# Kernel tuning notes

Measured on AMD Instinct MI355X. Metric: run time of the kernel, lower is better.

The kernel has to match this reference:

```python
import jax, jax.numpy as jnp
import numpy as np

N, E = 50000, 1600000
F_IN, EDGE_DIM, HID, HEADS, NCLS = 64, 16, 128, 4, 40
C = HID // HEADS  # per-head dim = 32


def setup_inputs() -> dict:
    key = jax.random.key(0)
    ks = jax.random.split(key, 20)
    s = 0.1
    inp = {
        'x': jax.random.normal(ks[0], (N, F_IN), jnp.float32),
        'edge_index': jax.random.randint(ks[1], (2, E), 0, N, jnp.int64),
        'edge_attr': jax.random.normal(ks[2], (E, EDGE_DIM), jnp.float32),
        # layer 1 params
        'W1': jax.random.normal(ks[3], (HID, F_IN), jnp.float32) * s,
        'as1': jax.random.normal(ks[4], (HEADS, C), jnp.float32) * s,
        'ad1': jax.random.normal(ks[5], (HEADS, C), jnp.float32) * s,
        'ae1': jax.random.normal(ks[6], (HEADS, C), jnp.float32) * s,
        'We1': jax.random.normal(ks[7], (HID, EDGE_DIM), jnp.float32) * s,
        'b1': jnp.zeros((HID,), jnp.float32),
        # layer 2 params
        'W2': jax.random.normal(ks[8], (HID, HID), jnp.float32) * s,
        'as2': jax.random.normal(ks[9], (HEADS, C), jnp.float32) * s,
        'ad2': jax.random.normal(ks[10], (HEADS, C), jnp.float32) * s,
        'ae2': jax.random.normal(ks[11], (HEADS, C), jnp.float32) * s,
        'We2': jax.random.normal(ks[12], (HID, EDGE_DIM), jnp.float32) * s,
        'b2': jnp.zeros((HID,), jnp.float32),
        # final classifier
        'Wlin': jax.random.normal(ks[13], (NCLS, HID), jnp.float32) * s,
        'blin': jnp.zeros((NCLS,), jnp.float32),
    }
    return inp


def gat_conv(x, src, dst, eattr, W, a_s, a_d, a_e, We, b):
    """PyG GATConv (concat=True, add_self_loops=True, fill_value='mean'), eval mode."""
    n = x.shape[0]
    H, Cd = a_s.shape
    h = (x @ W.T).reshape(n, H, Cd)  # [N,H,C]
    # self-loop edge_attr = per-destination mean of incoming edge_attr
    cnt = jax.ops.segment_sum(jnp.ones((dst.shape[0],), eattr.dtype), dst, num_segments=n)
    mean_ea = jax.ops.segment_sum(eattr, dst, num_segments=n) / jnp.maximum(cnt, 1.0)[:, None]
    loops = jnp.arange(n, dtype=src.dtype)
    s_idx = jnp.concatenate([src, loops])
    d_idx = jnp.concatenate([dst, loops])
    ea = jnp.concatenate([eattr, mean_ea], axis=0)  # [E+N, edge_dim]
    e = (ea @ We.T).reshape(-1, H, Cd)
    # edge-wise attention logits
    alpha = (h * a_s).sum(-1)[s_idx] + (h * a_d).sum(-1)[d_idx] + (e * a_e).sum(-1)  # [E+N,H]
    alpha = jax.nn.leaky_relu(alpha, 0.2)
    # segment softmax over destination neighborhoods (every node has a self-loop)
    amax = jax.ops.segment_max(alpha, d_idx, num_segments=n)
    ex = jnp.exp(alpha - amax[d_idx])
    den = jax.ops.segment_sum(ex, d_idx, num_segments=n)
    coef = ex / (den[d_idx] + 1e-16)
    out = jax.ops.segment_sum(h[s_idx] * coef[:, :, None], d_idx, num_segments=n)
    return out.reshape(n, H * Cd) + b


def reference(x, edge_index, edge_attr, W1, as1, ad1, ae1, We1, b1,
              W2, as2, ad2, ae2, We2, b2, Wlin, blin):
    src, dst = edge_index[0], edge_index[1]
    h = jax.nn.relu(gat_conv(x, src, dst, edge_attr, W1, as1, ad1, ae1, We1, b1))
    h = jax.nn.relu(gat_conv(h, src, dst, edge_attr, W2, as2, ad2, ae2, We2, b2))
    logits = h @ Wlin.T + blin
    return jax.nn.log_softmax(logits, axis=1)
```

## Files before the change

### kernel.cpp

```cpp
#include <hip/hip_runtime.h>
#include <hip/hip_bf16.h>
#include <math.h>


#define CHUNK 2048

typedef __attribute__((ext_vector_type(8))) short short8;
typedef __attribute__((ext_vector_type(4))) float floatx4;
typedef __attribute__((ext_vector_type(2))) float floatx2;

__device__ __forceinline__ unsigned short f2bf(float f) {
  unsigned u = __float_as_uint(f);
  unsigned r = u + 0x7FFFu + ((u >> 16) & 1u);
  return (unsigned short)(r >> 16);
}
__device__ __forceinline__ float bf2f(unsigned short b) {
  return __uint_as_float(((unsigned)b) << 16);
}

__global__ __launch_bounds__(512) void hist_kernel(const int* __restrict__ dst,
                                                   int* __restrict__ bucketCnt,
                                                   int E, int NB) {
  __shared__ int hist[512];
  const int tid = threadIdx.x;
  hist[tid] = 0;
  __syncthreads();
  const int e0 = blockIdx.x * CHUNK, e1 = min(e0 + CHUNK, E);
  for (int e = e0 + tid; e < e1; e += 512) atomicAdd(&hist[dst[e] >> 7], 1);
  __syncthreads();
  if (tid < NB && hist[tid]) atomicAdd(&bucketCnt[tid], hist[tid]);
}

__global__ __launch_bounds__(512) void scanB_kernel(const int* __restrict__ bucketCnt,
                                                    int* __restrict__ bucketOffs,
                                                    int* __restrict__ bucketPos,
                                                    int* __restrict__ offs,
                                                    int NB, int N, int E) {
  __shared__ int sc[512];
  const int tid = threadIdx.x;
  const int v = (tid < NB) ? bucketCnt[tid] : 0;
  sc[tid] = v;
  __syncthreads();
  for (int off = 1; off < 512; off <<= 1) {
    int t = (tid >= off) ? sc[tid - off] : 0;
    __syncthreads();
    sc[tid] += t;
    __syncthreads();
  }
  const int excl = sc[tid] - v;
  if (tid < NB) { bucketOffs[tid] = excl; bucketPos[tid] = excl; }
  if (tid == 0) { bucketOffs[NB] = E; offs[N] = E; }
}

__global__ __launch_bounds__(512) void partB_kernel(const int* __restrict__ src,
                                                    const int* __restrict__ dst,
                                                    const float* __restrict__ ea,
                                                    const float* __restrict__ ae1,
                                                    const float* __restrict__ We1,
                                                    const float* __restrict__ ae2,
                                                    const float* __restrict__ We2,
                                                    int* __restrict__ bucketPos,
                                                    int4* __restrict__ binned16,
                                                    int* __restrict__ binned4,
                                                    unsigned char* __restrict__ dlArr,
                                                    int E, int NB) {
  __shared__ float wa[128];
  __shared__ int hist[512], sc[512], lbase[513], gbase[512], lcnt[512];
  __shared__ int4 stg16[CHUNK];
  __shared__ int stg4[CHUNK];
  __shared__ unsigned char stg1[CHUNK];
  const int tid = threadIdx.x;
  const int e0 = blockIdx.x * CHUNK;
  const int e1 = min(e0 + CHUNK, E);
  hist[tid] = 0; lcnt[tid] = 0;
  if (tid < 128) {
    const float* aev = (tid < 64) ? ae1 : ae2;
    const float* Wev = (tid < 64) ? We1 : We2;
    const int h = (tid >> 4) & 3;
    const int d = tid & 15;
    float s = 0.f;
#pragma unroll
    for (int c = 0; c < 32; ++c) s += aev[h * 32 + c] * Wev[(h * 32 + c) * 16 + d];
    wa[tid] = s;
  }
  __syncthreads();
  for (int e = e0 + tid; e < e1; e += 512) atomicAdd(&hist[dst[e] >> 7], 1);
  __syncthreads();
  sc[tid] = hist[tid];
  __syncthreads();
  for (int off = 1; off < 512; off <<= 1) {
    int t = (tid >= off) ? sc[tid - off] : 0;
    __syncthreads();
    sc[tid] += t;
    __syncthreads();
  }
  lbase[tid + 1] = sc[tid];
  if (tid == 0) lbase[0] = 0;
  if (tid < NB && hist[tid] > 0) gbase[tid] = atomicAdd(&bucketPos[tid], hist[tid]);
  __syncthreads();
  for (int e = e0 + tid; e < e1; e += 512) {
    const int d = dst[e];
    const int b = d >> 7;
    const int lr = atomicAdd(&lcnt[b], 1);
    const float4* p = (const float4*)(ea + (size_t)e * 16);
    float4 q0 = p[0], q1 = p[1], q2 = p[2], q3 = p[3];
    float v16[16] = {q0.x, q0.y, q0.z, q0.w, q1.x, q1.y, q1.z, q1.w,
                     q2.x, q2.y, q2.z, q2.w, q3.x, q3.y, q3.z, q3.w};
    unsigned short rr[8];
#pragma unroll
    for (int h = 0; h < 8; ++h) {
      float s = 0.f;
#pragma unroll
      for (int d2 = 0; d2 < 16; ++d2) s += v16[d2] * wa[h * 16 + d2];
      rr[h] = f2bf(s);
    }
    int4 v;
    v.x = (src[e] & 0xFFFF) | ((d & 127) << 16);
    v.y = (int)(((unsigned)rr[1] << 16) | rr[0]);
    v.z = (int)(((unsigned)rr[3] << 16) | rr[2]);
    v.w = (int)(((unsigned)rr[5] << 16) | rr[4]);
    const int sp = lbase[b] + lr;
    stg16[sp] = v;
    stg4[sp] = (int)(((unsigned)rr[7] << 16) | rr[6]);
    stg1[sp] = (unsigned char)(d & 127);
  }
  __syncthreads();
  const int total = e1 - e0;
  for (int t = tid; t < total; t += 512) {
    int lo = 0, hi = 511;
    while (lo < hi) {
      int mid = (lo + hi + 1) >> 1;
      if (lbase[mid] <= t) lo = mid; else hi = mid - 1;
    }
    const int g = gbase[lo] + (t - lbase[lo]);
    binned16[g] = stg16[t];
    binned4[g] = stg4[t];
    dlArr[g] = stg1[t];
  }
}

__global__ __launch_bounds__(256) void passC_kernel(const int4* __restrict__ binned16,
                                                    const int* __restrict__ binned4,
                                                    const unsigned char* __restrict__ dlArr,
                                                    const int* __restrict__ bucketOffs,
                                                    int* __restrict__ srcS,
                                                    uint2* __restrict__ aeS1,
                                                    uint2* __restrict__ aeS2,
                                                    int* __restrict__ offs, int N) {
  __shared__ int cnt[128], dbase[129], dpos[128];
  const int tid = threadIdx.x;
  const int b = blockIdx.x;
  const int bo = bucketOffs[b], be = bucketOffs[b + 1];
  const int m = be - bo;
  if (tid < 128) { cnt[tid] = 0; dpos[tid] = 0; }
  __syncthreads();
  for (int t = tid; t < m; t += 256) atomicAdd(&cnt[dlArr[bo + t]], 1);
  __syncthreads();
  for (int off = 1; off < 128; off <<= 1) {
    int t = (tid < 128 && tid >= (unsigned)off) ? cnt[tid - off] : 0;
    __syncthreads();
    if (tid < 128) cnt[tid] += t;
    __syncthreads();
  }
  if (tid == 0) dbase[0] = 0;
  if (tid < 128) dbase[tid + 1] = cnt[tid];
  __syncthreads();
  const int dcnt = min(128, N - (b << 7));
  if (tid < dcnt) offs[(b << 7) + tid] = bo + dbase[tid];
  for (int t = tid; t < m; t += 256) {
    const int4 v = binned16[bo + t];
    const int w4 = binned4[bo + t];
    const int dl = (v.x >> 16) & 127;
    const int p = dbase[dl] + atomicAdd(&dpos[dl], 1);
    srcS[bo + p] = v.x & 0xFFFF;
    aeS1[bo + p] = make_uint2((unsigned)v.y, (unsigned)v.z);
    aeS2[bo + p] = make_uint2((unsigned)v.w, (unsigned)w4);
  }
}

__global__ __launch_bounds__(256) void cvtall_kernel(const float* __restrict__ W1,
                                                     unsigned short* __restrict__ Wb1,
                                                     const float* __restrict__ W2,
                                                     unsigned short* __restrict__ Wb2,
                                                     const float* __restrict__ Wlin,
                                                     unsigned short* __restrict__ whi,
                                                     unsigned short* __restrict__ wlo) {
  const int n1 = 128 * 64, n2 = 128 * 128, n3 = 48 * 128;
  int i = blockIdx.x * 256 + threadIdx.x;
  if (i < n1) {
    Wb1[i] = f2bf(W1[i]);
  } else if (i < n1 + n2) {
    Wb2[i - n1] = f2bf(W2[i - n1]);
  } else if (i < n1 + n2 + n3) {
    const int j = i - n1 - n2;
    float v = (j < 40 * 128) ? Wlin[j] : 0.f;
    unsigned short h = f2bf(v);
    whi[j] = h;
    wlo[j] = f2bf(v - bf2f(h));
  }
}

#define GEMM_MFMA_SWAPPED(KTOT, PA, PB)                                            \
  {                                                                                \
    for (int kc = 0; kc < (KTOT); kc += 32) {                                      \
      const int koff = kc + (quad << 3);                                           \
      short8 aw[2], bx[4];                                                         \
      _Pragma("unroll") for (int ct = 0; ct < 2; ++ct)                             \
        aw[ct] = *(const short8*)(&Bs[(w * 32 + ct * 16 + l15) * (PB) + koff]);    \
      _Pragma("unroll") for (int nt_ = 0; nt_ < 4; ++nt_)                          \
        bx[nt_] = *(const short8*)(&As[(nt_ * 16 + l15) * (PA) + koff]);           \
      _Pragma("unroll") for (int ct = 0; ct < 2; ++ct)                             \
        _Pragma("unroll") for (int nt_ = 0; nt_ < 4; ++nt_)                        \
          acc[ct][nt_] =                                                           \
              __builtin_amdgcn_mfma_f32_16x16x32_bf16(aw[ct], bx[nt_],             \
                                                      acc[ct][nt_], 0, 0, 0);      \
    }                                                                              \
  }

#define GEMM_WRITE_H_SWAPPED()                                                     \
  {                                                                                \
    _Pragma("unroll") for (int nt_ = 0; nt_ < 4; ++nt_) {                          \
      const int node = m0 + nt_ * 16 + l15;                                        \
      if (node < n) {                                                              \
        _Pragma("unroll") for (int ct = 0; ct < 2; ++ct) {                         \
          const int ch = w * 32 + ct * 16 + (quad << 2);                           \
          ushort4 o;                                                               \
          o.x = f2bf(acc[ct][nt_][0]); o.y = f2bf(acc[ct][nt_][1]);                \
          o.z = f2bf(acc[ct][nt_][2]); o.w = f2bf(acc[ct][nt_][3]);                \
          *(ushort4*)(H + (size_t)node * 128 + ch) = o;                            \
        }                                                                          \
      }                                                                            \
    }                                                                              \
  }

#define GEMM_SCORE_SWAPPED()                                                       \
  {                                                                                \
    float asv[2][4], adv[2][4];                                                    \
    _Pragma("unroll") for (int ct = 0; ct < 2; ++ct)                               \
      _Pragma("unroll") for (int r = 0; r < 4; ++r) {                              \
        const int c = w * 32 + ct * 16 + (quad << 2) + r;                          \
        asv[ct][r] = a_s[c]; adv[ct][r] = a_d[c];                                  \
      }                                                                            \
    _Pragma("unroll") for (int nt_ = 0; nt_ < 4; ++nt_) {                          \
      float ps = 0.f, pd = 0.f;                                                    \
      _Pragma("unroll") for (int ct = 0; ct < 2; ++ct)                             \
        _Pragma("unroll") for (int r = 0; r < 4; ++r) {                            \
          ps += acc[ct][nt_][r] * asv[ct][r];                                      \
          pd += acc[ct][nt_][r] * adv[ct][r];                                      \
        }                                                                          \
      ps += __shfl_xor(ps, 16); ps += __shfl_xor(ps, 32);                          \
      pd += __shfl_xor(pd, 16); pd += __shfl_xor(pd, 32);                          \
      if (lane < 16) {                                                             \
        const int node = m0 + nt_ * 16 + lane;                                     \
        if (node < n) {                                                            \
          ssc[(size_t)node * 4 + w] = ps;                                          \
          dsc[(size_t)node * 4 + w] = pd;                                          \
        }                                                                          \
      }                                                                            \
    }                                                                              \
  }

__global__ __launch_bounds__(256) void gemm_score_f32_kernel(const float* __restrict__ X,
                                                             const unsigned short* __restrict__ Wb,
                                                             const float* __restrict__ a_s,
                                                             const float* __restrict__ a_d,
                                                             unsigned short* __restrict__ H,
                                                             float* __restrict__ ssc,
                                                             float* __restrict__ dsc,
                                                             int n) {
  __shared__ unsigned short As[64 * 72];
  __shared__ unsigned short Bs[128 * 72];
  const int tid = threadIdx.x;
  const int w = tid >> 6;
  const int lane = tid & 63;
  const int m0 = blockIdx.x * 64;
  const int quad = lane >> 4;
  const int l15 = lane & 15;

#pragma unroll
  for (int it = 0; it < 4; ++it) {
    const int idx = it * 256 + tid;
    const int row = idx >> 4;
    const int c4 = (idx & 15) * 4;
    const int grow = min(m0 + row, n - 1);
    const float4 q = *(const float4*)(X + (size_t)grow * 64 + c4);
    unsigned short* dstp = &As[row * 72 + c4];
    dstp[0] = f2bf(q.x); dstp[1] = f2bf(q.y); dstp[2] = f2bf(q.z); dstp[3] = f2bf(q.w);
  }
#pragma unroll
  for (int it = 0; it < 4; ++it) {
    const int idx = it * 256 + tid;
    const int row = idx >> 3;
    const int c8 = (idx & 7) * 8;
    short8 v = *(const short8*)(Wb + (size_t)row * 64 + c8);
    *(short8*)(&Bs[row * 72 + c8]) = v;
  }
  __syncthreads();

  floatx4 acc[2][4];
#pragma unroll
  for (int ct = 0; ct < 2; ++ct)
#pragma unroll
    for (int nt_ = 0; nt_ < 4; ++nt_) acc[ct][nt_] = (floatx4)(0.f);

  GEMM_MFMA_SWAPPED(64, 72, 72)
  GEMM_WRITE_H_SWAPPED()
  GEMM_SCORE_SWAPPED()
}

__global__ __launch_bounds__(256) void gemm_score_kernel(const unsigned short* __restrict__ X,
                                                         const unsigned short* __restrict__ Wb,
                                                         const float* __restrict__ a_s,
                                                         const float* __restrict__ a_d,
                                                         unsigned short* __restrict__ H,
                                                         float* __restrict__ ssc,
                                                         float* __restrict__ dsc,
                                                         int n) {
  __shared__ unsigned short As[64 * 136];
  __shared__ unsigned short Bs[128 * 136];
  const int tid = threadIdx.x;
  const int w = tid >> 6;
  const int lane = tid & 63;
  const int m0 = blockIdx.x * 64;
  const int quad = lane >> 4;
  const int l15 = lane & 15;

#pragma unroll
  for (int it = 0; it < 4; ++it) {
    const int idx = it * 256 + tid;
    const int row = idx >> 4;
    const int c8 = (idx & 15) * 8;
    const int grow = min(m0 + row, n - 1);
    short8 v = *(const short8*)(X + (size_t)grow * 128 + c8);
    *(short8*)(&As[row * 136 + c8]) = v;
  }
#pragma unroll
  for (int it = 0; it < 8; ++it) {
    const int idx = it * 256 + tid;
    const int row = idx >> 4;
    const int c8 = (idx & 15) * 8;
    short8 v = *(const short8*)(Wb + (size_t)row * 128 + c8);
    *(short8*)(&Bs[row * 136 + c8]) = v;
  }
  __syncthreads();

  floatx4 acc[2][4];
#pragma unroll
  for (int ct = 0; ct < 2; ++ct)
#pragma unroll
    for (int nt_ = 0; nt_ < 4; ++nt_) acc[ct][nt_] = (floatx4)(0.f);

  GEMM_MFMA_SWAPPED(128, 136, 136)
  GEMM_WRITE_H_SWAPPED()
  GEMM_SCORE_SWAPPED()
}

__device__ __forceinline__ float leaky02(float a) { return a > 0.f ? a : 0.2f * a; }
__device__ __forceinline__ float sel4(float4 v, int h) {
  return (h == 0) ? v.x : (h == 1) ? v.y : (h == 2) ? v.z : v.w;
}

__global__ __launch_bounds__(256) void agg_kernel(const unsigned short* __restrict__ hin,
                                                  const float* __restrict__ ssc,
                                                  const float* __restrict__ dsc,
                                                  const unsigned short* __restrict__ aeS,
                                                  const int* __restrict__ offs,
                                                  const int* __restrict__ srcS,
                                                  const float* __restrict__ bias,
                                                  unsigned short* __restrict__ hout, int n) {
  __shared__ int sbuf[4][64];
  __shared__ float pbuf[4][256];
  const int tid = threadIdx.x;
  const int wv = tid >> 6;
  const int lane = tid & 63;
  const int node = blockIdx.x * 4 + wv;
  if (node >= n) return;
  const int l32 = lane & 31;
  const int half = lane >> 5;
  const int ch4 = l32 * 4;
  const int headB = l32 >> 3;
  const float4 dv = *(const float4*)(dsc + (size_t)node * 4);
  float4 l4 = make_float4(0.f, 0.f, 0.f, 0.f);
  float4 sa = make_float4(0.f, 0.f, 0.f, 0.f);
  floatx2 acc01 = (floatx2)(0.f);
  floatx2 acc23 = (floatx2)(0.f);
  const int j0 = offs[node], j1 = offs[node + 1];

  for (int jc = j0; jc < j1; jc += 64) {
    const int len = min(64, j1 - jc);
    float4 p4 = make_float4(0.f, 0.f, 0.f, 0.f);
    int sv = 0;
    if (lane < len) {
      const int j = jc + lane;
      sv = srcS[j];
      const ushort4 aq = *(const ushort4*)(aeS + (size_t)j * 4);
      const float4 ae4 = make_float4(bf2f(aq.x), bf2f(aq.y), bf2f(aq.z), bf2f(aq.w));
      const float4 ss4 = *(const float4*)(ssc + (size_t)sv * 4);
      sa.x += ae4.x; sa.y += ae4.y; sa.z += ae4.z; sa.w += ae4.w;
      p4.x = __expf(leaky02(ss4.x + dv.x + ae4.x));
      p4.y = __expf(leaky02(ss4.y + dv.y + ae4.y));
      p4.z = __expf(leaky02(ss4.z + dv.z + ae4.z));
      p4.w = __expf(leaky02(ss4.w + dv.w + ae4.w));
    }
    sbuf[wv][lane] = sv;
    *(float4*)(&pbuf[wv][lane * 4]) = p4;
    l4.x += p4.x; l4.y += p4.y; l4.z += p4.z; l4.w += p4.w;
    int k = 0;
    for (; k + 8 <= len; k += 8) {
      int s[4];
      float p[4];
      uint2 d[4];
#pragma unroll
      for (int u = 0; u < 4; ++u) {
        const int kk = k + 2 * u + half;
        s[u] = sbuf[wv][kk];
        p[u] = pbuf[wv][kk * 4 + headB];
      }
#pragma unroll
      for (int u = 0; u < 4; ++u)
        d[u] = *(const uint2*)(hin + (size_t)s[u] * 128 + ch4);
#pragma unroll
      for (int u = 0; u < 4; ++u) {
        floatx2 p2; p2.x = p[u]; p2.y = p[u];
        floatx2 h01, h23;
        h01.x = __uint_as_float(d[u].x << 16);
        h01.y = __uint_as_float(d[u].x & 0xFFFF0000u);
        h23.x = __uint_as_float(d[u].y << 16);
        h23.y = __uint_as_float(d[u].y & 0xFFFF0000u);
        acc01 += p2 * h01;
        acc23 += p2 * h23;
      }
    }
    for (; k < len; k += 2) {
      int kk = k + half;
      if (kk < len) {
        int s = sbuf[wv][kk];
        float p = pbuf[wv][kk * 4 + headB];
        uint2 d = *(const uint2*)(hin + (size_t)s * 128 + ch4);
        floatx2 p2; p2.x = p; p2.y = p;
        floatx2 h01, h23;
        h01.x = __uint_as_float(d.x << 16);
        h01.y = __uint_as_float(d.x & 0xFFFF0000u);
        h23.x = __uint_as_float(d.y << 16);
        h23.y = __uint_as_float(d.y & 0xFFFF0000u);
        acc01 += p2 * h01;
        acc23 += p2 * h23;
      }
    }
  }

  float acc[4] = {acc01.x, acc01.y, acc23.x, acc23.y};
#pragma unroll
  for (int off = 32; off; off >>= 1) {
    sa.x += __shfl_xor(sa.x, off);
    sa.y += __shfl_xor(sa.y, off);
    sa.z += __shfl_xor(sa.z, off);
    sa.w += __shfl_xor(sa.w, off);
    l4.x += __shfl_xor(l4.x, off);
    l4.y += __shfl_xor(l4.y, off);
    l4.z += __shfl_xor(l4.z, off);
    l4.w += __shfl_xor(l4.w, off);
  }
#pragma unroll
  for (int i = 0; i < 4; ++i) acc[i] += __shfl_xor(acc[i], 32);

  const int deg = j1 - j0;
  const float invd = 1.f / fmaxf((float)deg, 1.f);
  const float ssn = ssc[(size_t)node * 4 + headB];
  const float aloop = leaky02(ssn + sel4(dv, headB) + sel4(sa, headB) * invd);
  const float pl = __expf(aloop);
  const float lF = sel4(l4, headB) + pl;
  const uint2 hd = *(const uint2*)(hin + (size_t)node * 128 + ch4);
  const float hv0 = __uint_as_float(hd.x << 16);
  const float hv1 = __uint_as_float(hd.x & 0xFFFF0000u);
  const float hv2 = __uint_as_float(hd.y << 16);
  const float hv3 = __uint_as_float(hd.y & 0xFFFF0000u);
  const float inv = 1.f / (lF + 1e-16f);
  const float4 bi = *(const float4*)(bias + ch4);
  const float o0 = fmaxf((acc[0] + pl * hv0) * inv + bi.x, 0.f);
  const float o1 = fmaxf((acc[1] + pl * hv1) * inv + bi.y, 0.f);
  const float o2 = fmaxf((acc[2] + pl * hv2) * inv + bi.z, 0.f);
  const float o3 = fmaxf((acc[3] + pl * hv3) * inv + bi.w, 0.f);
  if (half == 0) {
    ushort4 o;
    o.x = f2bf(o0); o.y = f2bf(o1); o.z = f2bf(o2); o.w = f2bf(o3);
    *(ushort4*)(hout + (size_t)node * 128 + ch4) = o;
  }
}

__global__ __launch_bounds__(256) void classifier_kernel(const unsigned short* __restrict__ h,
                                                         const unsigned short* __restrict__ Whi,
                                                         const unsigned short* __restrict__ Wlo,
                                                         const float* __restrict__ blin,
                                                         float* __restrict__ out, int n) {
  const int w = threadIdx.x >> 6;
  const int lane = threadIdx.x & 63;
  const int quad = lane >> 4;
  const int l15 = lane & 15;
  const int row0 = blockIdx.x * 64 + w * 16;
  if (row0 >= n) return;
  int rowm = row0 + l15;
  if (rowm >= n) rowm = n - 1;
  floatx4 acc[3];
#pragma unroll
  for (int nt = 0; nt < 3; ++nt) acc[nt] = (floatx4)(0.f);
  const size_t hbase = (size_t)rowm * 128;
#pragma unroll
  for (int kc = 0; kc < 128; kc += 32) {
    const int koff = kc + (quad << 3);
    short8 a = *(const short8*)(h + hbase + koff);
#pragma unroll
    for (int nt = 0; nt < 3; ++nt) {
      short8 bh = *(const short8*)(Whi + (size_t)(nt * 16 + l15) * 128 + koff);
      short8 bl = *(const short8*)(Wlo + (size_t)(nt * 16 + l15) * 128 + koff);
      acc[nt] = __builtin_amdgcn_mfma_f32_16x16x32_bf16(a, bh, acc[nt], 0, 0, 0);
      acc[nt] = __builtin_amdgcn_mfma_f32_16x16x32_bf16(a, bl, acc[nt], 0, 0, 0);
    }
  }
  const float bl0 = blin[l15];
  const float bl1 = blin[16 + l15];
  const float bl2 = (l15 < 8) ? blin[32 + l15] : 0.f;
#pragma unroll
  for (int r = 0; r < 4; ++r) {
    const int rrow = row0 + (quad << 2) + r;
    const float v0 = acc[0][r] + bl0;
    const float v1 = acc[1][r] + bl1;
    const float v2 = (l15 < 8) ? (acc[2][r] + bl2) : -INFINITY;
    float m = fmaxf(v0, fmaxf(v1, v2));
#pragma unroll
    for (int off = 8; off; off >>= 1) m = fmaxf(m, __shfl_xor(m, off, 16));
    const float e2 = (l15 < 8) ? __expf(v2 - m) : 0.f;
    float s = __expf(v0 - m) + __expf(v1 - m) + e2;
#pragma unroll
    for (int off = 8; off; off >>= 1) s += __shfl_xor(s, off, 16);
    const float ls = m + __logf(s);
    if (rrow < n) {
      float* po = out + (size_t)rrow * 40;
      po[l15] = v0 - ls;
      po[16 + l15] = v1 - ls;
      if (l15 < 8) po[32 + l15] = v2 - ls;
    }
  }
}

extern "C" void kernel_launch(void* const* d_in, const int* in_sizes, int n_in,
                              void* d_out, int out_size, void* d_ws, size_t ws_size,
                              hipStream_t stream) {
  const float* x    = (const float*)d_in[0];
  const int*   eidx = (const int*)d_in[1];
  const float* ea   = (const float*)d_in[2];
  const float* W1   = (const float*)d_in[3];
  const float* as1  = (const float*)d_in[4];
  const float* ad1  = (const float*)d_in[5];
  const float* ae1w = (const float*)d_in[6];
  const float* We1  = (const float*)d_in[7];
  const float* b1   = (const float*)d_in[8];
  const float* W2   = (const float*)d_in[9];
  const float* as2  = (const float*)d_in[10];
  const float* ad2  = (const float*)d_in[11];
  const float* ae2w = (const float*)d_in[12];
  const float* We2  = (const float*)d_in[13];
  const float* b2   = (const float*)d_in[14];
  const float* Wlin = (const float*)d_in[15];
  const float* blin = (const float*)d_in[16];
  float* out = (float*)d_out;

  const int N = in_sizes[0] / 64;
  const int E = in_sizes[1] / 2;
  const int* src = eidx;
  const int* dst = eidx + E;
  const int NB = (N + 127) >> 7;

  char* wsb = (char*)d_ws;
  size_t off = 0;
  auto alloc = [&](size_t bytes) -> void* {
    void* p = wsb + off;
    off = (off + bytes + 255) & ~(size_t)255;
    return p;
  };
  int* bucketCnt  = (int*)alloc(512 * 4);
  int* bucketOffs = (int*)alloc(513 * 4);
  int* bucketPos  = (int*)alloc(512 * 4);
  int* offs       = (int*)alloc((size_t)(N + 1) * 4);
  uint2* aeS1     = (uint2*)alloc((size_t)E * 8);
  uint2* aeS2     = (uint2*)alloc((size_t)E * 8);
  void* regC      = alloc((size_t)E * 16);
  int4* binned16  = (int4*)regC;
  unsigned short* hA = (unsigned short*)regC;
  int* binned4    = (int*)alloc((size_t)E * 4);
  unsigned char* dlArr = (unsigned char*)alloc((size_t)E);
  int* srcS       = (int*)alloc((size_t)E * 4);
  unsigned short* Wb1 = (unsigned short*)alloc(128 * 64 * 2);
  unsigned short* Wb2 = (unsigned short*)alloc(128 * 128 * 2);
  unsigned short* Wlh = (unsigned short*)alloc(48 * 128 * 2);
  unsigned short* Wll = (unsigned short*)alloc(48 * 128 * 2);
  float* ssc      = (float*)alloc((size_t)N * 4 * 4);
  float* dsc      = (float*)alloc((size_t)N * 4 * 4);
  unsigned short* hB = (unsigned short*)alloc((size_t)N * 128 * 2);

  const int gg = (N + 63) / 64;
  const int gs = (N + 3) / 4;
  const int gp = (E + CHUNK - 1) / CHUNK;
  const int ncvt = 128 * 64 + 128 * 128 + 48 * 128;

  hipMemsetAsync(bucketCnt, 0, 512 * 4, stream);
  hist_kernel<<<gp, 512, 0, stream>>>(dst, bucketCnt, E, NB);
  scanB_kernel<<<1, 512, 0, stream>>>(bucketCnt, bucketOffs, bucketPos, offs, NB, N, E);
  partB_kernel<<<gp, 512, 0, stream>>>(src, dst, ea, ae1w, We1, ae2w, We2, bucketPos,
                                       binned16, binned4, dlArr, E, NB);
  passC_kernel<<<NB, 256, 0, stream>>>(binned16, binned4, dlArr, bucketOffs, srcS,
                                       aeS1, aeS2, offs, N);

  cvtall_kernel<<<(ncvt + 255) / 256, 256, 0, stream>>>(W1, Wb1, W2, Wb2, Wlin, Wlh, Wll);

  gemm_score_f32_kernel<<<gg, 256, 0, stream>>>(x, Wb1, as1, ad1, hA, ssc, dsc, N);
  agg_kernel<<<gs, 256, 0, stream>>>(hA, ssc, dsc, (const unsigned short*)aeS1, offs, srcS, b1, hB, N);

  gemm_score_kernel<<<gg, 256, 0, stream>>>(hB, Wb2, as2, ad2, hA, ssc, dsc, N);
  agg_kernel<<<gs, 256, 0, stream>>>(hA, ssc, dsc, (const unsigned short*)aeS2, offs, srcS, b2, hB, N);

  classifier_kernel<<<gg, 256, 0, stream>>>(hB, Wlh, Wll, blin, out, N);
}
```

Baseline: 464.6 us.

## Reuse per-chunk histograms in partition kernel and encode bucket in packed edge

The histogram kernel now writes each chunk's per-bucket counts to global memory, so the partition kernel no longer recomputes the histogram from dst. The 512-entry block scan is replaced by a wave-level shuffle scan plus a per-wave offset sum, which removes most of the barriers. The bucket id is packed into the upper bits of the staged edge word, so the scatter phase reads it directly instead of binary-searching lbase, and the byte staging array is dropped. In exchange it adds a small global buffer write and read per chunk, and it relies on the bucket id fitting in 9 bits.

```diff
diff --git a/kernel.cpp b/kernel.cpp
--- a/kernel.cpp
+++ b/kernel.cpp
@@ -20,6 +20,7 @@
 
 __global__ __launch_bounds__(512) void hist_kernel(const int* __restrict__ dst,
                                                    int* __restrict__ bucketCnt,
+                                                   int* __restrict__ chunkHist,
                                                    int E, int NB) {
   __shared__ int hist[512];
   const int tid = threadIdx.x;
@@ -28,6 +29,7 @@
   const int e0 = blockIdx.x * CHUNK, e1 = min(e0 + CHUNK, E);
   for (int e = e0 + tid; e < e1; e += 512) atomicAdd(&hist[dst[e] >> 7], 1);
   __syncthreads();
+  chunkHist[(size_t)blockIdx.x * 512 + tid] = hist[tid];
   if (tid < NB && hist[tid]) atomicAdd(&bucketCnt[tid], hist[tid]);
 }
 
@@ -59,20 +61,23 @@
                                                     const float* __restrict__ We1,
                                                     const float* __restrict__ ae2,
                                                     const float* __restrict__ We2,
+                                                    const int* __restrict__ chunkHist,
                                                     int* __restrict__ bucketPos,
                                                     int4* __restrict__ binned16,
                                                     int* __restrict__ binned4,
                                                     unsigned char* __restrict__ dlArr,
                                                     int E, int NB) {
   __shared__ float wa[128];
-  __shared__ int hist[512], sc[512], lbase[513], gbase[512], lcnt[512];
+  __shared__ int lbase[513], gbase[512], lcnt[512];
+  __shared__ int waveSum[8];
   __shared__ int4 stg16[CHUNK];
   __shared__ int stg4[CHUNK];
-  __shared__ unsigned char stg1[CHUNK];
   const int tid = threadIdx.x;
+  const int wv = tid >> 6;
+  const int lane = tid & 63;
   const int e0 = blockIdx.x * CHUNK;
   const int e1 = min(e0 + CHUNK, E);
-  hist[tid] = 0; lcnt[tid] = 0;
+  lcnt[tid] = 0;
   if (tid < 128) {
     const float* aev = (tid < 64) ? ae1 : ae2;
     const float* Wev = (tid < 64) ? We1 : We2;
@@ -83,20 +88,22 @@
     for (int c = 0; c < 32; ++c) s += aev[h * 32 + c] * Wev[(h * 32 + c) * 16 + d];
     wa[tid] = s;
   }
-  __syncthreads();
-  for (int e = e0 + tid; e < e1; e += 512) atomicAdd(&hist[dst[e] >> 7], 1);
-  __syncthreads();
-  sc[tid] = hist[tid];
-  __syncthreads();
-  for (int off = 1; off < 512; off <<= 1) {
-    int t = (tid >= off) ? sc[tid - off] : 0;
-    __syncthreads();
-    sc[tid] += t;
-    __syncthreads();
-  }
-  lbase[tid + 1] = sc[tid];
+  const int hv = chunkHist[(size_t)blockIdx.x * 512 + tid];
+  int v = hv;
+#pragma unroll
+  for (int off = 1; off < 64; off <<= 1) {
+    int t = __shfl_up(v, off);
+    if (lane >= off) v += t;
+  }
+  if (lane == 63) waveSum[wv] = v;
+  __syncthreads();
+  int woff = 0;
+#pragma unroll
+  for (int i = 0; i < 8; ++i) woff += (i < wv) ? waveSum[i] : 0;
+  const int incl = v + woff;
+  lbase[tid + 1] = incl;
   if (tid == 0) lbase[0] = 0;
-  if (tid < NB && hist[tid] > 0) gbase[tid] = atomicAdd(&bucketPos[tid], hist[tid]);
+  if (tid < NB && hv > 0) gbase[tid] = atomicAdd(&bucketPos[tid], hv);
   __syncthreads();
   for (int e = e0 + tid; e < e1; e += 512) {
     const int d = dst[e];
@@ -109,33 +116,30 @@
     unsigned short rr[8];
 #pragma unroll
     for (int h = 0; h < 8; ++h) {
-      float s = 0.f;
-#pragma unroll
-      for (int d2 = 0; d2 < 16; ++d2) s += v16[d2] * wa[h * 16 + d2];
-      rr[h] = f2bf(s);
+      float sm = 0.f;
+#pragma unroll
+      for (int d2 = 0; d2 < 16; ++d2) sm += v16[d2] * wa[h * 16 + d2];
+      rr[h] = f2bf(sm);
     }
-    int4 v;
-    v.x = (src[e] & 0xFFFF) | ((d & 127) << 16);
-    v.y = (int)(((unsigned)rr[1] << 16) | rr[0]);
-    v.z = (int)(((unsigned)rr[3] << 16) | rr[2]);
-    v.w = (int)(((unsigned)rr[5] << 16) | rr[4]);
+    int4 pv;
+    pv.x = (int)(((unsigned)(src[e] & 0xFFFF)) | ((unsigned)(d & 127) << 16) |
+                 ((unsigned)b << 23));
+    pv.y = (int)(((unsigned)rr[1] << 16) | rr[0]);
+    pv.z = (int)(((unsigned)rr[3] << 16) | rr[2]);
+    pv.w = (int)(((unsigned)rr[5] << 16) | rr[4]);
     const int sp = lbase[b] + lr;
-    stg16[sp] = v;
+    stg16[sp] = pv;
     stg4[sp] = (int)(((unsigned)rr[7] << 16) | rr[6]);
-    stg1[sp] = (unsigned char)(d & 127);
   }
   __syncthreads();
   const int total = e1 - e0;
   for (int t = tid; t < total; t += 512) {
-    int lo = 0, hi = 511;
-    while (lo < hi) {
-      int mid = (lo + hi + 1) >> 1;
-      if (lbase[mid] <= t) lo = mid; else hi = mid - 1;
-    }
-    const int g = gbase[lo] + (t - lbase[lo]);
-    binned16[g] = stg16[t];
+    const int4 pv = stg16[t];
+    const int b = (int)(((unsigned)pv.x) >> 23);
+    const int g = gbase[b] + (t - lbase[b]);
+    binned16[g] = pv;
     binned4[g] = stg4[t];
-    dlArr[g] = stg1[t];
+    dlArr[g] = (unsigned char)((pv.x >> 16) & 127);
   }
 }
 
@@ -570,6 +574,7 @@
   const int* src = eidx;
   const int* dst = eidx + E;
   const int NB = (N + 127) >> 7;
+  const int gp = (E + CHUNK - 1) / CHUNK;
 
   char* wsb = (char*)d_ws;
   size_t off = 0;
@@ -582,6 +587,7 @@
   int* bucketOffs = (int*)alloc(513 * 4);
   int* bucketPos  = (int*)alloc(512 * 4);
   int* offs       = (int*)alloc((size_t)(N + 1) * 4);
+  int* chunkHist  = (int*)alloc((size_t)gp * 512 * 4);
   uint2* aeS1     = (uint2*)alloc((size_t)E * 8);
   uint2* aeS2     = (uint2*)alloc((size_t)E * 8);
   void* regC      = alloc((size_t)E * 16);
@@ -600,14 +606,13 @@
 
   const int gg = (N + 63) / 64;
   const int gs = (N + 3) / 4;
-  const int gp = (E + CHUNK - 1) / CHUNK;
   const int ncvt = 128 * 64 + 128 * 128 + 48 * 128;
 
   hipMemsetAsync(bucketCnt, 0, 512 * 4, stream);
-  hist_kernel<<<gp, 512, 0, stream>>>(dst, bucketCnt, E, NB);
+  hist_kernel<<<gp, 512, 0, stream>>>(dst, bucketCnt, chunkHist, E, NB);
   scanB_kernel<<<1, 512, 0, stream>>>(bucketCnt, bucketOffs, bucketPos, offs, NB, N, E);
-  partB_kernel<<<gp, 512, 0, stream>>>(src, dst, ea, ae1w, We1, ae2w, We2, bucketPos,
-                                       binned16, binned4, dlArr, E, NB);
+  partB_kernel<<<gp, 512, 0, stream>>>(src, dst, ea, ae1w, We1, ae2w, We2, chunkHist,
+                                       bucketPos, binned16, binned4, dlArr, E, NB);
   passC_kernel<<<NB, 256, 0, stream>>>(binned16, binned4, dlArr, bucketOffs, srcS,
                                        aeS1, aeS2, offs, N);
 
```

After: 458.1 us. Within noise of the previous version (-1.4%).
